# Kernel tuning notes

Hardware: AMD Instinct MI355X
Metric: run time of the kernel (lower is better)

The kernel has to match this reference:

```python
import jax, jax.numpy as jnp
import numpy as np

B, NQ, S, D = 2, 2048, 2048, 1024
H, HD, OUT = 16, 64, 1024


def setup_inputs() -> dict:
    key = jax.random.key(0)
    ks = jax.random.split(key, 8)
    scale = 1.0 / np.sqrt(D)
    return {
        "queries": jax.random.normal(ks[0], (B, NQ, D), jnp.float32),
        "keys": jax.random.normal(ks[1], (B, S, D), jnp.float32),
        "values": jax.random.normal(ks[2], (B, S, D), jnp.float32),
        "indicators": jax.random.uniform(ks[3], (B, S), jnp.float32),
        "Wq": jax.random.normal(ks[4], (D, H * HD), jnp.float32) * scale,
        "Wk": jax.random.normal(ks[5], (D, H * HD), jnp.float32) * scale,
        "Wv": jax.random.normal(ks[6], (D, H * HD), jnp.float32) * scale,
        "Wo": jax.random.normal(ks[7], (H * HD, OUT), jnp.float32) * scale,
    }


def reference(queries, keys, values, indicators, Wq, Wk, Wv, Wo):
    b, nq, _ = queries.shape
    s = keys.shape[1]
    # projections -> [b, len, H, HD] -> [b, H, len, HD]
    Q = (queries @ Wq).reshape(b, nq, H, HD).transpose(0, 2, 1, 3)
    K = (keys @ Wk).reshape(b, s, H, HD).transpose(0, 2, 1, 3)
    V = (values @ Wv).reshape(b, s, H, HD).transpose(0, 2, 1, 3)
    # scores [b, H, nq, s], softmax over s, THEN multiplicative mask
    scores = jnp.einsum("bhqd,bhkd->bhqk", Q, K) / jnp.sqrt(jnp.float32(HD))
    probs = jax.nn.softmax(scores, axis=-1)
    probs = probs * indicators[:, None, None, :]  # post-softmax mask
    ctx = jnp.einsum("bhqk,bhkd->bhqd", probs, V)
    ctx = ctx.transpose(0, 2, 1, 3).reshape(b, nq, H * HD)
    return ctx @ Wo
```

## Files before the change

kernel.cpp:

```cpp
#include <hip/hip_runtime.h>


typedef float f32x4 __attribute__((ext_vector_type(4)));
typedef __bf16 bf16x8 __attribute__((ext_vector_type(8)));
typedef __bf16 bf16x4 __attribute__((ext_vector_type(4)));

#define DEVINL __device__ __forceinline__

DEVINL void gll16(const void* g, void* l) {
  __builtin_amdgcn_global_load_lds((const __attribute__((address_space(1))) void*)g,
                                   (__attribute__((address_space(3))) void*)l, 16, 0, 0);
}
DEVINL bf16x8 ldfrag(const void* p) { return __builtin_bit_cast(bf16x8, *(const int4*)p); }
DEVINL f32x4 mfma16(bf16x8 a, bf16x8 b, f32x4 c) {
  return __builtin_amdgcn_mfma_f32_16x16x32_bf16(a, b, c, 0, 0, 0);
}

__global__ __launch_bounds__(256) void prep_k(
    const float* __restrict__ q, const float* __restrict__ k,
    const float* __restrict__ v, const float* __restrict__ Wq,
    const float* __restrict__ Wk, const float* __restrict__ Wv,
    const float* __restrict__ Wo, __bf16* __restrict__ qo, __bf16* __restrict__ ko,
    __bf16* __restrict__ vo, __bf16* __restrict__ o0, __bf16* __restrict__ o1,
    __bf16* __restrict__ o2, __bf16* __restrict__ o3) {
  const int bid = blockIdx.x;
  const int t = threadIdx.x;
  if (bid < 12288) {
    int plane = bid >> 12, bx = bid & 4095;
    const float* s = plane == 0 ? q : (plane == 1 ? k : v);
    __bf16* d = plane == 0 ? qo : (plane == 1 ? ko : vo);
    size_t i = ((size_t)bx * 256 + t) * 4;
    float4 f = *(const float4*)(s + i);
    bf16x4 o = {(__bf16)f.x, (__bf16)f.y, (__bf16)f.z, (__bf16)f.w};
    *(bf16x4*)(d + i) = o;
  } else {
    __shared__ float tl[32][33];
    int wid = bid - 12288;
    int z = wid >> 10, x = wid & 31, y = (wid >> 5) & 31;
    const float* W = z == 0 ? Wq : z == 1 ? Wk : z == 2 ? Wv : Wo;
    __bf16* o = z == 0 ? o0 : z == 1 ? o1 : z == 2 ? o2 : o3;
    float scale = z == 0 ? 0.125f * 1.44269504f : 1.0f;
    int c0 = x * 32, r0 = y * 32;
    int tx = t & 31, ty = t >> 5;
#pragma unroll
    for (int rr = 0; rr < 32; rr += 8)
      tl[rr + ty][tx] = W[(size_t)(r0 + rr + ty) * 1024 + c0 + tx];
    __syncthreads();
#pragma unroll
    for (int cc = 0; cc < 32; cc += 8)
      o[(size_t)(c0 + cc + ty) * 1024 + r0 + tx] = (__bf16)(tl[tx][cc + ty] * scale);
  }
}

template <int MT>
DEVINL void gemm_core(const __bf16* __restrict__ A, const __bf16* __restrict__ Bt,
                      int K, int m0, int n0, char* As, char* Bs, f32x4 (&acc)[MT][4],
                      int t) {
  const int lane = t & 63, wv = t >> 6;
  const int li = lane & 15, g = lane >> 4;
  const int wr = wv >> 1, wc = wv & 1;
  const size_t lda = (size_t)K * 2;
  for (int kt = 0; kt < K; kt += 32) {
    if (kt) __syncthreads();
#pragma unroll
    for (int p = 0; p < MT / 2; ++p) {
      int off = p * 4096 + t * 16;
      int row = off >> 6, ch = (off >> 4) & 3;
      int gch = ch ^ ((row >> 1) & 3);
      gll16((const char*)A + (size_t)(m0 + row) * lda + (size_t)kt * 2 + gch * 16,
            As + off);
    }
#pragma unroll
    for (int p = 0; p < 2; ++p) {
      int off = p * 4096 + t * 16;
      int row = off >> 6, ch = (off >> 4) & 3;
      int gch = ch ^ ((row >> 1) & 3);
      gll16((const char*)Bt + (size_t)(n0 + row) * lda + (size_t)kt * 2 + gch * 16,
            Bs + off);
    }
    __syncthreads();
    bf16x8 af[MT], bfr[4];
#pragma unroll
    for (int mt = 0; mt < MT; ++mt) {
      int row = wr * (MT * 16) + mt * 16 + li;
      int gch = g ^ ((row >> 1) & 3);
      af[mt] = ldfrag(As + row * 64 + gch * 16);
    }
#pragma unroll
    for (int nt = 0; nt < 4; ++nt) {
      int row = wc * 64 + nt * 16 + li;
      int gch = g ^ ((row >> 1) & 3);
      bfr[nt] = ldfrag(Bs + row * 64 + gch * 16);
    }
#pragma unroll
    for (int mt = 0; mt < MT; ++mt)
#pragma unroll
      for (int nt = 0; nt < 4; ++nt)
        acc[mt][nt] = mfma16(af[mt], bfr[nt], acc[mt][nt]);
  }
}

__global__ __launch_bounds__(256) void gemm_qkv(
    const __bf16* __restrict__ qb, const __bf16* __restrict__ kb,
    const __bf16* __restrict__ vb, const __bf16* __restrict__ WqT,
    const __bf16* __restrict__ WkT, const __bf16* __restrict__ WvT,
    const float* __restrict__ ind, __bf16* __restrict__ Qp, __bf16* __restrict__ Kp,
    __bf16* __restrict__ Vtp) {
  __shared__ __align__(16) char As[4 * 2048];
  __shared__ __align__(16) char Bs[8192];
  const int z = blockIdx.z;
  const __bf16* A = z == 0 ? qb : z == 1 ? kb : vb;
  const __bf16* Bt = z == 0 ? WqT : z == 1 ? WkT : WvT;
  const int m0 = blockIdx.y * 128, n0 = blockIdx.x * 128;
  f32x4 acc[4][4] = {};
  gemm_core<4>(A, Bt, 1024, m0, n0, As, Bs, acc, threadIdx.x);
  const int lane = threadIdx.x & 63, wv = threadIdx.x >> 6;
  const int li = lane & 15, g = lane >> 4;
  const int wr = wv >> 1, wc = wv & 1;
#pragma unroll
  for (int mt = 0; mt < 4; ++mt)
#pragma unroll
    for (int nt = 0; nt < 4; ++nt) {
      int m = m0 + wr * 64 + mt * 16 + g * 4;
      int n = n0 + wc * 64 + nt * 16 + li;
      if (z < 2) {
        __bf16* Cb = z ? Kp : Qp;
#pragma unroll
        for (int r = 0; r < 4; ++r)
          Cb[(size_t)(m + r) * 1024 + n] = (__bf16)acc[mt][nt][r];
      } else {
        float4 i4 = *(const float4*)(ind + m);
        bf16x4 o = {(__bf16)(acc[mt][nt][0] * i4.x), (__bf16)(acc[mt][nt][1] * i4.y),
                    (__bf16)(acc[mt][nt][2] * i4.z), (__bf16)(acc[mt][nt][3] * i4.w)};
        *(bf16x4*)(Vtp + (size_t)n * 4096 + m) = o;
      }
    }
}

__global__ __launch_bounds__(256) void gemm_out(const __bf16* __restrict__ ctx,
                                                const __bf16* __restrict__ WoT,
                                                float* __restrict__ out) {
  __shared__ __align__(16) char As[2 * 2048];
  __shared__ __align__(16) char Bs[8192];
  const int m0 = blockIdx.y * 64, n0 = blockIdx.x * 128;
  f32x4 acc[2][4] = {};
  gemm_core<2>(ctx, WoT, 1024, m0, n0, As, Bs, acc, threadIdx.x);
  const int lane = threadIdx.x & 63, wv = threadIdx.x >> 6;
  const int li = lane & 15, g = lane >> 4;
  const int wr = wv >> 1, wc = wv & 1;
#pragma unroll
  for (int mt = 0; mt < 2; ++mt)
#pragma unroll
    for (int nt = 0; nt < 4; ++nt) {
      int m = m0 + wr * 32 + mt * 16 + g * 4;
      int n = n0 + wc * 64 + nt * 16 + li;
#pragma unroll
      for (int r = 0; r < 4; ++r) out[(size_t)(m + r) * 1024 + n] = acc[mt][nt][r];
    }
}

__global__ __launch_bounds__(256) void flash_k(const __bf16* __restrict__ Qp,
                                               const __bf16* __restrict__ Kp,
                                               const __bf16* __restrict__ Vt,
                                               __bf16* __restrict__ ctx0,
                                               __bf16* __restrict__ ctx1,
                                               float* __restrict__ pl) {
  __shared__ __align__(16) char smem[35840];
  char* kv = smem;
  char* qps = smem + 16384;
  const int t = threadIdx.x;
  const int lane = t & 63, wv = t >> 6;
  const int li = lane & 15, g = lane >> 4;
  const int sp = blockIdx.x >> 9, rest = blockIdx.x & 511;
  const int qt = rest & 15, h = (rest >> 4) & 15, b = rest >> 8;
  const size_t qrow0 = (size_t)b * 2048 + (size_t)qt * 128;
  __bf16* ctx = sp ? ctx1 : ctx0;
  char* psw = qps + wv * 4864;

#pragma unroll
  for (int p = 0; p < 4; ++p) {
    int off = p * 4096 + t * 16;
    int row = off >> 7, ch = (off >> 4) & 7;
    int gch = ch ^ (row & 7);
    gll16((const char*)Qp + ((qrow0 + row) * 1024 + h * 64) * 2 + gch * 16, qps + off);
  }
  __syncthreads();

  bf16x8 qf[2][2];
#pragma unroll
  for (int nt = 0; nt < 2; ++nt)
#pragma unroll
    for (int ks = 0; ks < 2; ++ks) {
      int row = wv * 32 + nt * 16 + li;
      int gch = (4 * ks + g) ^ (row & 7);
      qf[nt][ks] = ldfrag(qps + row * 128 + gch * 16);
    }

  f32x4 acc[4][2] = {};
  float lsum[2] = {0.0f, 0.0f};

  for (int kt = sp * 16; kt < sp * 16 + 16; ++kt) {
    __syncthreads();
#pragma unroll
    for (int p = 0; p < 2; ++p) {
      int off = p * 4096 + t * 16;
      int row = off >> 7, ch = (off >> 4) & 7;
      int gch = ch ^ (row & 7);
      gll16((const char*)Kp +
                (((size_t)b * 2048 + kt * 64 + row) * 1024 + h * 64) * 2 + gch * 16,
            kv + off);
      gll16((const char*)Vt +
                ((size_t)(h * 64 + row) * 4096 + (size_t)b * 2048 + kt * 64) * 2 +
                gch * 16,
            kv + 8192 + off);
    }
    __syncthreads();

    f32x4 st[4][2] = {};
#pragma unroll
    for (int ks = 0; ks < 2; ++ks)
#pragma unroll
      for (int mt = 0; mt < 4; ++mt) {
        int row = mt * 16 + li;
        int gch = (4 * ks + g) ^ (row & 7);
        bf16x8 kf = ldfrag(kv + row * 128 + gch * 16);
        st[mt][0] = mfma16(kf, qf[0][ks], st[mt][0]);
        st[mt][1] = mfma16(kf, qf[1][ks], st[mt][1]);
      }

#pragma unroll
    for (int nt = 0; nt < 2; ++nt) {
      float rs = 0.0f;
#pragma unroll
      for (int mt = 0; mt < 4; ++mt) {
        float p0 = __builtin_amdgcn_exp2f(st[mt][nt][0]);
        float p1 = __builtin_amdgcn_exp2f(st[mt][nt][1]);
        float p2 = __builtin_amdgcn_exp2f(st[mt][nt][2]);
        float p3 = __builtin_amdgcn_exp2f(st[mt][nt][3]);
        rs += (p0 + p1) + (p2 + p3);
        bf16x4 pv = {(__bf16)p0, (__bf16)p1, (__bf16)p2, (__bf16)p3};
        *(bf16x4*)(psw + (nt * 16 + li) * 152 + mt * 32 + g * 8) = pv;
      }
      lsum[nt] += rs;
    }

#pragma unroll
    for (int kc = 0; kc < 2; ++kc) {
      bf16x8 pf0 = ldfrag(psw + li * 152 + kc * 64 + g * 16);
      bf16x8 pf1 = ldfrag(psw + (16 + li) * 152 + kc * 64 + g * 16);
#pragma unroll
      for (int mtd = 0; mtd < 4; ++mtd) {
        int row = mtd * 16 + li;
        int gch = (4 * kc + g) ^ (row & 7);
        bf16x8 vf = ldfrag(kv + 8192 + row * 128 + gch * 16);
        acc[mtd][0] = mfma16(vf, pf0, acc[mtd][0]);
        acc[mtd][1] = mfma16(vf, pf1, acc[mtd][1]);
      }
    }
  }

#pragma unroll
  for (int nt = 0; nt < 2; ++nt) {
    float l = lsum[nt];
    l += __shfl_xor(l, 16);
    l += __shfl_xor(l, 32);
    float linv = 1.0f / l;
    size_t qrow = qrow0 + wv * 32 + nt * 16 + li;
    if (g == 0) pl[((size_t)sp * 4096 + qrow) * 16 + h] = l;
#pragma unroll
    for (int mtd = 0; mtd < 4; ++mtd) {
      bf16x4 o = {(__bf16)(acc[mtd][nt][0] * linv), (__bf16)(acc[mtd][nt][1] * linv),
                  (__bf16)(acc[mtd][nt][2] * linv), (__bf16)(acc[mtd][nt][3] * linv)};
      *(bf16x4*)(ctx + qrow * 1024 + h * 64 + mtd * 16 + g * 4) = o;
    }
  }
}

__global__ __launch_bounds__(256) void combine_k(const __bf16* __restrict__ c0,
                                                 const __bf16* __restrict__ c1,
                                                 const float* __restrict__ pl,
                                                 __bf16* __restrict__ ctx) {
  size_t e = ((size_t)blockIdx.x * 256 + threadIdx.x) * 8;
  int qrow = (int)(e >> 10), h = ((int)e & 1023) >> 6;
  float l0 = pl[(size_t)qrow * 16 + h];
  float l1 = pl[(size_t)(4096 + qrow) * 16 + h];
  float w = 1.0f / (l0 + l1);
  float w0 = l0 * w, w1 = l1 * w;
  bf16x8 a = *(const bf16x8*)(c0 + e);
  bf16x8 b = *(const bf16x8*)(c1 + e);
  bf16x8 o;
#pragma unroll
  for (int i = 0; i < 8; ++i) o[i] = (__bf16)((float)a[i] * w0 + (float)b[i] * w1);
  *(bf16x8*)(ctx + e) = o;
}

extern "C" void kernel_launch(void* const* d_in, const int* in_sizes, int n_in,
                              void* d_out, int out_size, void* d_ws, size_t ws_size,
                              hipStream_t stream) {
  const float* q = (const float*)d_in[0];
  const float* k = (const float*)d_in[1];
  const float* v = (const float*)d_in[2];
  const float* ind = (const float*)d_in[3];
  const float* Wq = (const float*)d_in[4];
  const float* Wk = (const float*)d_in[5];
  const float* Wv = (const float*)d_in[6];
  const float* Wo = (const float*)d_in[7];
  char* ws = (char*)d_ws;
  const size_t MB = 1024 * 1024;
  __bf16* qb = (__bf16*)(ws + 0);
  __bf16* kb = (__bf16*)(ws + 8 * MB);
  __bf16* vb = (__bf16*)(ws + 16 * MB);
  __bf16* WqT = (__bf16*)(ws + 24 * MB);
  __bf16* WkT = (__bf16*)(ws + 26 * MB);
  __bf16* WvT = (__bf16*)(ws + 28 * MB);
  __bf16* WoT = (__bf16*)(ws + 30 * MB);
  __bf16* Qp = (__bf16*)(ws + 32 * MB);
  __bf16* Kp = (__bf16*)(ws + 40 * MB);
  __bf16* Vtp = (__bf16*)(ws + 48 * MB);
  __bf16* ctx0 = (__bf16*)(ws + 0);
  __bf16* ctx1 = (__bf16*)(ws + 8 * MB);
  __bf16* ctx = (__bf16*)(ws + 16 * MB);
  float* pl = (float*)(ws + 24 * MB);
  float* out = (float*)d_out;

  prep_k<<<dim3(16384), 256, 0, stream>>>(q, k, v, Wq, Wk, Wv, Wo, qb, kb, vb, WqT,
                                          WkT, WvT, WoT);
  gemm_qkv<<<dim3(8, 32, 3), 256, 0, stream>>>(qb, kb, vb, WqT, WkT, WvT, ind, Qp, Kp,
                                               Vtp);
  flash_k<<<dim3(1024), 256, 0, stream>>>(Qp, Kp, Vtp, ctx0, ctx1, pl);
  combine_k<<<dim3(2048), 256, 0, stream>>>(ctx0, ctx1, pl, ctx);
  gemm_out<<<dim3(8, 64), 256, 0, stream>>>(ctx, WoT, out);
}
```

Before: 238.4 us.

## Deepen GEMM K-tile to 64, stage V-transpose through LDS, enlarge out-proj tiles

The shared GEMM core now loads a 64-wide K slice per iteration with an 8-way XOR swizzle. This halves the number of barrier and load rounds and doubles the MFMAs issued per sync. The V projection epilogue writes its transposed, mask-scaled output into an LDS staging tile and then stores 16-byte contiguous rows to global memory, replacing scattered 8-byte strided stores. The output projection moves from 64x128 to 128x128 tiles, which improves reuse but halves the grid to 256 blocks and raises LDS use per block to 32KB.

```diff
diff --git a/kernel.cpp b/kernel.cpp
--- a/kernel.cpp
+++ b/kernel.cpp
@@ -52,51 +52,56 @@
   }
 }
 
-template <int MT>
-DEVINL void gemm_core(const __bf16* __restrict__ A, const __bf16* __restrict__ Bt,
-                      int K, int m0, int n0, char* As, char* Bs, f32x4 (&acc)[MT][4],
-                      int t) {
+DEVINL void gemm_core64(const __bf16* __restrict__ A, const __bf16* __restrict__ Bt,
+                        int K, int m0, int n0, char* As, char* Bs, f32x4 (&acc)[4][4],
+                        int t) {
   const int lane = t & 63, wv = t >> 6;
   const int li = lane & 15, g = lane >> 4;
   const int wr = wv >> 1, wc = wv & 1;
   const size_t lda = (size_t)K * 2;
-  for (int kt = 0; kt < K; kt += 32) {
+  for (int kt = 0; kt < K; kt += 64) {
     if (kt) __syncthreads();
 #pragma unroll
-    for (int p = 0; p < MT / 2; ++p) {
+    for (int p = 0; p < 4; ++p) {
       int off = p * 4096 + t * 16;
-      int row = off >> 6, ch = (off >> 4) & 3;
-      int gch = ch ^ ((row >> 1) & 3);
+      int row = off >> 7, ch = (off >> 4) & 7;
+      int gch = ch ^ (row & 7);
       gll16((const char*)A + (size_t)(m0 + row) * lda + (size_t)kt * 2 + gch * 16,
             As + off);
     }
 #pragma unroll
-    for (int p = 0; p < 2; ++p) {
+    for (int p = 0; p < 4; ++p) {
       int off = p * 4096 + t * 16;
-      int row = off >> 6, ch = (off >> 4) & 3;
-      int gch = ch ^ ((row >> 1) & 3);
+      int row = off >> 7, ch = (off >> 4) & 7;
+      int gch = ch ^ (row & 7);
       gll16((const char*)Bt + (size_t)(n0 + row) * lda + (size_t)kt * 2 + gch * 16,
             Bs + off);
     }
     __syncthreads();
-    bf16x8 af[MT], bfr[4];
-#pragma unroll
-    for (int mt = 0; mt < MT; ++mt) {
-      int row = wr * (MT * 16) + mt * 16 + li;
-      int gch = g ^ ((row >> 1) & 3);
-      af[mt] = ldfrag(As + row * 64 + gch * 16);
-    }
-#pragma unroll
-    for (int nt = 0; nt < 4; ++nt) {
-      int row = wc * 64 + nt * 16 + li;
-      int gch = g ^ ((row >> 1) & 3);
-      bfr[nt] = ldfrag(Bs + row * 64 + gch * 16);
-    }
-#pragma unroll
-    for (int mt = 0; mt < MT; ++mt)
-#pragma unroll
-      for (int nt = 0; nt < 4; ++nt)
-        acc[mt][nt] = mfma16(af[mt], bfr[nt], acc[mt][nt]);
+    bf16x8 af[4][2], bfr[4][2];
+#pragma unroll
+    for (int mt = 0; mt < 4; ++mt)
+#pragma unroll
+      for (int ks = 0; ks < 2; ++ks) {
+        int row = wr * 64 + mt * 16 + li;
+        int gch = (ks * 4 + g) ^ (row & 7);
+        af[mt][ks] = ldfrag(As + row * 128 + gch * 16);
+      }
+#pragma unroll
+    for (int nt = 0; nt < 4; ++nt)
+#pragma unroll
+      for (int ks = 0; ks < 2; ++ks) {
+        int row = wc * 64 + nt * 16 + li;
+        int gch = (ks * 4 + g) ^ (row & 7);
+        bfr[nt][ks] = ldfrag(Bs + row * 128 + gch * 16);
+      }
+#pragma unroll
+    for (int ks = 0; ks < 2; ++ks)
+#pragma unroll
+      for (int mt = 0; mt < 4; ++mt)
+#pragma unroll
+        for (int nt = 0; nt < 4; ++nt)
+          acc[mt][nt] = mfma16(af[mt][ks], bfr[nt][ks], acc[mt][nt]);
   }
 }
 
@@ -106,14 +111,73 @@
     const __bf16* __restrict__ WkT, const __bf16* __restrict__ WvT,
     const float* __restrict__ ind, __bf16* __restrict__ Qp, __bf16* __restrict__ Kp,
     __bf16* __restrict__ Vtp) {
-  __shared__ __align__(16) char As[4 * 2048];
-  __shared__ __align__(16) char Bs[8192];
+  __shared__ __align__(16) char smem[32768];
+  char* As = smem;
+  char* Bs = smem + 16384;
   const int z = blockIdx.z;
   const __bf16* A = z == 0 ? qb : z == 1 ? kb : vb;
   const __bf16* Bt = z == 0 ? WqT : z == 1 ? WkT : WvT;
   const int m0 = blockIdx.y * 128, n0 = blockIdx.x * 128;
   f32x4 acc[4][4] = {};
-  gemm_core<4>(A, Bt, 1024, m0, n0, As, Bs, acc, threadIdx.x);
+  gemm_core64(A, Bt, 1024, m0, n0, As, Bs, acc, threadIdx.x);
+  const int t = threadIdx.x;
+  const int lane = t & 63, wv = t >> 6;
+  const int li = lane & 15, g = lane >> 4;
+  const int wr = wv >> 1, wc = wv & 1;
+  if (z < 2) {
+    __bf16* Cb = z ? Kp : Qp;
+#pragma unroll
+    for (int mt = 0; mt < 4; ++mt)
+#pragma unroll
+      for (int nt = 0; nt < 4; ++nt) {
+        int m = m0 + wr * 64 + mt * 16 + g * 4;
+        int n = n0 + wc * 64 + nt * 16 + li;
+#pragma unroll
+        for (int r = 0; r < 4; ++r)
+          Cb[(size_t)(m + r) * 1024 + n] = (__bf16)acc[mt][nt][r];
+      }
+  } else {
+    char* Tt = smem;
+    float4 iv[4];
+#pragma unroll
+    for (int mt = 0; mt < 4; ++mt)
+      iv[mt] = *(const float4*)(ind + m0 + wr * 64 + mt * 16 + g * 4);
+#pragma unroll
+    for (int h2 = 0; h2 < 2; ++h2) {
+      __syncthreads();
+      if (wc == h2) {
+#pragma unroll
+        for (int mt = 0; mt < 4; ++mt)
+#pragma unroll
+          for (int nt = 0; nt < 4; ++nt) {
+            bf16x4 o = {(__bf16)(acc[mt][nt][0] * iv[mt].x),
+                        (__bf16)(acc[mt][nt][1] * iv[mt].y),
+                        (__bf16)(acc[mt][nt][2] * iv[mt].z),
+                        (__bf16)(acc[mt][nt][3] * iv[mt].w)};
+            *(bf16x4*)(Tt + (nt * 16 + li) * 272 + (wr * 64 + mt * 16 + g * 4) * 2) = o;
+          }
+      }
+      __syncthreads();
+      int nl = t >> 2, part = t & 3;
+      const int4* src = (const int4*)(Tt + nl * 272 + part * 64);
+      int4 v0 = src[0], v1 = src[1], v2 = src[2], v3 = src[3];
+      int4* dst = (int4*)((char*)Vtp +
+                          ((size_t)(n0 + h2 * 64 + nl) * 4096 + m0 + part * 32) * 2);
+      dst[0] = v0;
+      dst[1] = v1;
+      dst[2] = v2;
+      dst[3] = v3;
+    }
+  }
+}
+
+__global__ __launch_bounds__(256) void gemm_out(const __bf16* __restrict__ ctx,
+                                                const __bf16* __restrict__ WoT,
+                                                float* __restrict__ out) {
+  __shared__ __align__(16) char smem[32768];
+  const int m0 = blockIdx.y * 128, n0 = blockIdx.x * 128;
+  f32x4 acc[4][4] = {};
+  gemm_core64(ctx, WoT, 1024, m0, n0, smem, smem + 16384, acc, threadIdx.x);
   const int lane = threadIdx.x & 63, wv = threadIdx.x >> 6;
   const int li = lane & 15, g = lane >> 4;
   const int wr = wv >> 1, wc = wv & 1;
@@ -122,37 +186,6 @@
 #pragma unroll
     for (int nt = 0; nt < 4; ++nt) {
       int m = m0 + wr * 64 + mt * 16 + g * 4;
-      int n = n0 + wc * 64 + nt * 16 + li;
-      if (z < 2) {
-        __bf16* Cb = z ? Kp : Qp;
-#pragma unroll
-        for (int r = 0; r < 4; ++r)
-          Cb[(size_t)(m + r) * 1024 + n] = (__bf16)acc[mt][nt][r];
-      } else {
-        float4 i4 = *(const float4*)(ind + m);
-        bf16x4 o = {(__bf16)(acc[mt][nt][0] * i4.x), (__bf16)(acc[mt][nt][1] * i4.y),
-                    (__bf16)(acc[mt][nt][2] * i4.z), (__bf16)(acc[mt][nt][3] * i4.w)};
-        *(bf16x4*)(Vtp + (size_t)n * 4096 + m) = o;
-      }
-    }
-}
-
-__global__ __launch_bounds__(256) void gemm_out(const __bf16* __restrict__ ctx,
-                                                const __bf16* __restrict__ WoT,
-                                                float* __restrict__ out) {
-  __shared__ __align__(16) char As[2 * 2048];
-  __shared__ __align__(16) char Bs[8192];
-  const int m0 = blockIdx.y * 64, n0 = blockIdx.x * 128;
-  f32x4 acc[2][4] = {};
-  gemm_core<2>(ctx, WoT, 1024, m0, n0, As, Bs, acc, threadIdx.x);
-  const int lane = threadIdx.x & 63, wv = threadIdx.x >> 6;
-  const int li = lane & 15, g = lane >> 4;
-  const int wr = wv >> 1, wc = wv & 1;
-#pragma unroll
-  for (int mt = 0; mt < 2; ++mt)
-#pragma unroll
-    for (int nt = 0; nt < 4; ++nt) {
-      int m = m0 + wr * 32 + mt * 16 + g * 4;
       int n = n0 + wc * 64 + nt * 16 + li;
 #pragma unroll
       for (int r = 0; r < 4; ++r) out[(size_t)(m + r) * 1024 + n] = acc[mt][nt][r];
@@ -329,5 +362,5 @@
                                                Vtp);
   flash_k<<<dim3(1024), 256, 0, stream>>>(Qp, Kp, Vtp, ctx0, ctx1, pl);
   combine_k<<<dim3(2048), 256, 0, stream>>>(ctx0, ctx1, pl, ctx);
-  gemm_out<<<dim3(8, 64), 256, 0, stream>>>(ctx, WoT, out);
-}
+  gemm_out<<<dim3(8, 32), 256, 0, stream>>>(ctx, WoT, out);
+}
```

New measurement: 245.0 us. +2.8%, slower.

## Fuse fp32-to-bf16 activation conversion into QKV projection GEMM loads

Applied to the files above, without the earlier changes.

Removes the separate pass that converts queries/keys/values from fp32 to bf16. The QKV GEMM now loads fp32 tiles straight into LDS with an 8-chunk XOR swizzle and converts to bf16 while building MFMA fragments. This avoids writing and rereading 48MB of bf16 intermediates. In exchange the GEMM reads twice as many A bytes per tile, uses more LDS, and does conversion work on every tile reload (each A tile is reread by 8 column blocks). gemm_core is inlined into both GEMMs.

```diff
diff --git a/kernel.cpp b/kernel.cpp
--- a/kernel.cpp
+++ b/kernel.cpp
@@ -12,62 +12,58 @@
                                    (__attribute__((address_space(3))) void*)l, 16, 0, 0);
 }
 DEVINL bf16x8 ldfrag(const void* p) { return __builtin_bit_cast(bf16x8, *(const int4*)p); }
+DEVINL f32x4 ldfrag_f(const void* p) { return __builtin_bit_cast(f32x4, *(const int4*)p); }
 DEVINL f32x4 mfma16(bf16x8 a, bf16x8 b, f32x4 c) {
   return __builtin_amdgcn_mfma_f32_16x16x32_bf16(a, b, c, 0, 0, 0);
 }
 
 __global__ __launch_bounds__(256) void prep_k(
-    const float* __restrict__ q, const float* __restrict__ k,
-    const float* __restrict__ v, const float* __restrict__ Wq,
-    const float* __restrict__ Wk, const float* __restrict__ Wv,
-    const float* __restrict__ Wo, __bf16* __restrict__ qo, __bf16* __restrict__ ko,
-    __bf16* __restrict__ vo, __bf16* __restrict__ o0, __bf16* __restrict__ o1,
-    __bf16* __restrict__ o2, __bf16* __restrict__ o3) {
-  const int bid = blockIdx.x;
+    const float* __restrict__ Wq, const float* __restrict__ Wk,
+    const float* __restrict__ Wv, const float* __restrict__ Wo,
+    __bf16* __restrict__ o0, __bf16* __restrict__ o1, __bf16* __restrict__ o2,
+    __bf16* __restrict__ o3) {
+  __shared__ float tl[32][33];
   const int t = threadIdx.x;
-  if (bid < 12288) {
-    int plane = bid >> 12, bx = bid & 4095;
-    const float* s = plane == 0 ? q : (plane == 1 ? k : v);
-    __bf16* d = plane == 0 ? qo : (plane == 1 ? ko : vo);
-    size_t i = ((size_t)bx * 256 + t) * 4;
-    float4 f = *(const float4*)(s + i);
-    bf16x4 o = {(__bf16)f.x, (__bf16)f.y, (__bf16)f.z, (__bf16)f.w};
-    *(bf16x4*)(d + i) = o;
-  } else {
-    __shared__ float tl[32][33];
-    int wid = bid - 12288;
-    int z = wid >> 10, x = wid & 31, y = (wid >> 5) & 31;
-    const float* W = z == 0 ? Wq : z == 1 ? Wk : z == 2 ? Wv : Wo;
-    __bf16* o = z == 0 ? o0 : z == 1 ? o1 : z == 2 ? o2 : o3;
-    float scale = z == 0 ? 0.125f * 1.44269504f : 1.0f;
-    int c0 = x * 32, r0 = y * 32;
-    int tx = t & 31, ty = t >> 5;
-#pragma unroll
-    for (int rr = 0; rr < 32; rr += 8)
-      tl[rr + ty][tx] = W[(size_t)(r0 + rr + ty) * 1024 + c0 + tx];
-    __syncthreads();
-#pragma unroll
-    for (int cc = 0; cc < 32; cc += 8)
-      o[(size_t)(c0 + cc + ty) * 1024 + r0 + tx] = (__bf16)(tl[tx][cc + ty] * scale);
-  }
-}
-
-template <int MT>
-DEVINL void gemm_core(const __bf16* __restrict__ A, const __bf16* __restrict__ Bt,
-                      int K, int m0, int n0, char* As, char* Bs, f32x4 (&acc)[MT][4],
-                      int t) {
+  int z = blockIdx.x >> 10, x = blockIdx.x & 31, y = (blockIdx.x >> 5) & 31;
+  const float* W = z == 0 ? Wq : z == 1 ? Wk : z == 2 ? Wv : Wo;
+  __bf16* o = z == 0 ? o0 : z == 1 ? o1 : z == 2 ? o2 : o3;
+  float scale = z == 0 ? 0.125f * 1.44269504f : 1.0f;
+  int c0 = x * 32, r0 = y * 32;
+  int tx = t & 31, ty = t >> 5;
+#pragma unroll
+  for (int rr = 0; rr < 32; rr += 8)
+    tl[rr + ty][tx] = W[(size_t)(r0 + rr + ty) * 1024 + c0 + tx];
+  __syncthreads();
+#pragma unroll
+  for (int cc = 0; cc < 32; cc += 8)
+    o[(size_t)(c0 + cc + ty) * 1024 + r0 + tx] = (__bf16)(tl[tx][cc + ty] * scale);
+}
+
+__global__ __launch_bounds__(256) void gemm_qkv(
+    const float* __restrict__ qf, const float* __restrict__ kf,
+    const float* __restrict__ vf, const __bf16* __restrict__ WqT,
+    const __bf16* __restrict__ WkT, const __bf16* __restrict__ WvT,
+    const float* __restrict__ ind, __bf16* __restrict__ Qp, __bf16* __restrict__ Kp,
+    __bf16* __restrict__ Vtp) {
+  __shared__ __align__(16) char As[16384];
+  __shared__ __align__(16) char Bs[8192];
+  const int z = blockIdx.z;
+  const float* A = z == 0 ? qf : z == 1 ? kf : vf;
+  const __bf16* Bt = z == 0 ? WqT : z == 1 ? WkT : WvT;
+  const int m0 = blockIdx.y * 128, n0 = blockIdx.x * 128;
+  const int t = threadIdx.x;
   const int lane = t & 63, wv = t >> 6;
   const int li = lane & 15, g = lane >> 4;
   const int wr = wv >> 1, wc = wv & 1;
-  const size_t lda = (size_t)K * 2;
-  for (int kt = 0; kt < K; kt += 32) {
+  f32x4 acc[4][4] = {};
+  for (int kt = 0; kt < 1024; kt += 32) {
     if (kt) __syncthreads();
 #pragma unroll
-    for (int p = 0; p < MT / 2; ++p) {
+    for (int p = 0; p < 4; ++p) {
       int off = p * 4096 + t * 16;
-      int row = off >> 6, ch = (off >> 4) & 3;
-      int gch = ch ^ ((row >> 1) & 3);
-      gll16((const char*)A + (size_t)(m0 + row) * lda + (size_t)kt * 2 + gch * 16,
+      int row = off >> 7, ch = (off >> 4) & 7;
+      int gch = ch ^ (row & 7);
+      gll16((const char*)A + ((size_t)(m0 + row) * 1024 + kt) * 4 + gch * 16,
             As + off);
     }
 #pragma unroll
@@ -75,16 +71,20 @@
       int off = p * 4096 + t * 16;
       int row = off >> 6, ch = (off >> 4) & 3;
       int gch = ch ^ ((row >> 1) & 3);
-      gll16((const char*)Bt + (size_t)(n0 + row) * lda + (size_t)kt * 2 + gch * 16,
+      gll16((const char*)Bt + ((size_t)(n0 + row) * 1024 + kt) * 2 + gch * 16,
             Bs + off);
     }
     __syncthreads();
-    bf16x8 af[MT], bfr[4];
-#pragma unroll
-    for (int mt = 0; mt < MT; ++mt) {
-      int row = wr * (MT * 16) + mt * 16 + li;
-      int gch = g ^ ((row >> 1) & 3);
-      af[mt] = ldfrag(As + row * 64 + gch * 16);
+    bf16x8 af[4], bfr[4];
+#pragma unroll
+    for (int mt = 0; mt < 4; ++mt) {
+      int row = wr * 64 + mt * 16 + li;
+      int c0 = (2 * g) ^ (row & 7), c1 = (2 * g + 1) ^ (row & 7);
+      f32x4 lo = ldfrag_f(As + row * 128 + c0 * 16);
+      f32x4 hi = ldfrag_f(As + row * 128 + c1 * 16);
+      bf16x8 o = {(__bf16)lo[0], (__bf16)lo[1], (__bf16)lo[2], (__bf16)lo[3],
+                  (__bf16)hi[0], (__bf16)hi[1], (__bf16)hi[2], (__bf16)hi[3]};
+      af[mt] = o;
     }
 #pragma unroll
     for (int nt = 0; nt < 4; ++nt) {
@@ -93,30 +93,11 @@
       bfr[nt] = ldfrag(Bs + row * 64 + gch * 16);
     }
 #pragma unroll
-    for (int mt = 0; mt < MT; ++mt)
+    for (int mt = 0; mt < 4; ++mt)
 #pragma unroll
       for (int nt = 0; nt < 4; ++nt)
         acc[mt][nt] = mfma16(af[mt], bfr[nt], acc[mt][nt]);
   }
-}
-
-__global__ __launch_bounds__(256) void gemm_qkv(
-    const __bf16* __restrict__ qb, const __bf16* __restrict__ kb,
-    const __bf16* __restrict__ vb, const __bf16* __restrict__ WqT,
-    const __bf16* __restrict__ WkT, const __bf16* __restrict__ WvT,
-    const float* __restrict__ ind, __bf16* __restrict__ Qp, __bf16* __restrict__ Kp,
-    __bf16* __restrict__ Vtp) {
-  __shared__ __align__(16) char As[4 * 2048];
-  __shared__ __align__(16) char Bs[8192];
-  const int z = blockIdx.z;
-  const __bf16* A = z == 0 ? qb : z == 1 ? kb : vb;
-  const __bf16* Bt = z == 0 ? WqT : z == 1 ? WkT : WvT;
-  const int m0 = blockIdx.y * 128, n0 = blockIdx.x * 128;
-  f32x4 acc[4][4] = {};
-  gemm_core<4>(A, Bt, 1024, m0, n0, As, Bs, acc, threadIdx.x);
-  const int lane = threadIdx.x & 63, wv = threadIdx.x >> 6;
-  const int li = lane & 15, g = lane >> 4;
-  const int wr = wv >> 1, wc = wv & 1;
 #pragma unroll
   for (int mt = 0; mt < 4; ++mt)
 #pragma unroll
@@ -140,14 +121,51 @@
 __global__ __launch_bounds__(256) void gemm_out(const __bf16* __restrict__ ctx,
                                                 const __bf16* __restrict__ WoT,
                                                 float* __restrict__ out) {
-  __shared__ __align__(16) char As[2 * 2048];
+  __shared__ __align__(16) char As[4096];
   __shared__ __align__(16) char Bs[8192];
+  const int t = threadIdx.x;
+  const int lane = t & 63, wv = t >> 6;
+  const int li = lane & 15, g = lane >> 4;
+  const int wr = wv >> 1, wc = wv & 1;
   const int m0 = blockIdx.y * 64, n0 = blockIdx.x * 128;
   f32x4 acc[2][4] = {};
-  gemm_core<2>(ctx, WoT, 1024, m0, n0, As, Bs, acc, threadIdx.x);
-  const int lane = threadIdx.x & 63, wv = threadIdx.x >> 6;
-  const int li = lane & 15, g = lane >> 4;
-  const int wr = wv >> 1, wc = wv & 1;
+  for (int kt = 0; kt < 1024; kt += 32) {
+    if (kt) __syncthreads();
+    {
+      int off = t * 16;
+      int row = off >> 6, ch = (off >> 4) & 3;
+      int gch = ch ^ ((row >> 1) & 3);
+      gll16((const char*)ctx + ((size_t)(m0 + row) * 1024 + kt) * 2 + gch * 16,
+            As + off);
+    }
+#pragma unroll
+    for (int p = 0; p < 2; ++p) {
+      int off = p * 4096 + t * 16;
+      int row = off >> 6, ch = (off >> 4) & 3;
+      int gch = ch ^ ((row >> 1) & 3);
+      gll16((const char*)WoT + ((size_t)(n0 + row) * 1024 + kt) * 2 + gch * 16,
+            Bs + off);
+    }
+    __syncthreads();
+    bf16x8 af[2], bfr[4];
+#pragma unroll
+    for (int mt = 0; mt < 2; ++mt) {
+      int row = wr * 32 + mt * 16 + li;
+      int gch = g ^ ((row >> 1) & 3);
+      af[mt] = ldfrag(As + row * 64 + gch * 16);
+    }
+#pragma unroll
+    for (int nt = 0; nt < 4; ++nt) {
+      int row = wc * 64 + nt * 16 + li;
+      int gch = g ^ ((row >> 1) & 3);
+      bfr[nt] = ldfrag(Bs + row * 64 + gch * 16);
+    }
+#pragma unroll
+    for (int mt = 0; mt < 2; ++mt)
+#pragma unroll
+      for (int nt = 0; nt < 4; ++nt)
+        acc[mt][nt] = mfma16(af[mt], bfr[nt], acc[mt][nt]);
+  }
 #pragma unroll
   for (int mt = 0; mt < 2; ++mt)
 #pragma unroll
@@ -307,9 +325,6 @@
   const float* Wo = (const float*)d_in[7];
   char* ws = (char*)d_ws;
   const size_t MB = 1024 * 1024;
-  __bf16* qb = (__bf16*)(ws + 0);
-  __bf16* kb = (__bf16*)(ws + 8 * MB);
-  __bf16* vb = (__bf16*)(ws + 16 * MB);
   __bf16* WqT = (__bf16*)(ws + 24 * MB);
   __bf16* WkT = (__bf16*)(ws + 26 * MB);
   __bf16* WvT = (__bf16*)(ws + 28 * MB);
@@ -323,9 +338,8 @@
   float* pl = (float*)(ws + 24 * MB);
   float* out = (float*)d_out;
 
-  prep_k<<<dim3(16384), 256, 0, stream>>>(q, k, v, Wq, Wk, Wv, Wo, qb, kb, vb, WqT,
-                                          WkT, WvT, WoT);
-  gemm_qkv<<<dim3(8, 32, 3), 256, 0, stream>>>(qb, kb, vb, WqT, WkT, WvT, ind, Qp, Kp,
+  prep_k<<<dim3(4096), 256, 0, stream>>>(Wq, Wk, Wv, Wo, WqT, WkT, WvT, WoT);
+  gemm_qkv<<<dim3(8, 32, 3), 256, 0, stream>>>(q, k, v, WqT, WkT, WvT, ind, Qp, Kp,
                                                Vtp);
   flash_k<<<dim3(1024), 256, 0, stream>>>(Qp, Kp, Vtp, ctx0, ctx1, pl);
   combine_k<<<dim3(2048), 256, 0, stream>>>(ctx0, ctx1, pl, ctx);
```

New measurement: 252.3 us. 1.06x slower.
